# Optimization experiments

Hardware: AMD Instinct MI355X
Metric: run time of the kernel (lower is better)

The kernel has to match this reference:

```python
import jax, jax.numpy as jnp
import numpy as np

NUM_TREES = 256
DEPTH = 6
TREE_DIM = 2
INPUT_DIM = 256
BATCH = 2048


def sparsemax(x, axis=0):
    # Euclidean projection onto the simplex along `axis`.
    x = jnp.moveaxis(x, axis, -1)
    z = jnp.flip(jnp.sort(x, axis=-1), axis=-1)           # descending
    cz = jnp.cumsum(z, axis=-1)
    k = jnp.arange(1, x.shape[-1] + 1, dtype=x.dtype)
    support = (1.0 + k * z) > cz                          # boolean support set
    k_sel = jnp.sum(support, axis=-1, keepdims=True)      # |S(z)|
    tau = (jnp.take_along_axis(cz, k_sel - 1, axis=-1) - 1.0) / k_sel.astype(x.dtype)
    out = jnp.maximum(x - tau, 0.0)
    return jnp.moveaxis(out, -1, axis)


def sparsemoid(x):
    return jnp.clip(0.5 * x + 0.5, 0.0, 1.0)


def make_bin_codes(depth):
    idx = np.arange(2 ** depth)
    offs = 2 ** np.arange(depth)
    bc = ((idx[None, :] // offs[:, None]) % 2).astype(np.float32)  # [depth, 2^depth]
    return jnp.asarray(np.stack([bc, 1.0 - bc], axis=-1))          # [depth, 2^depth, 2]


def setup_inputs() -> dict:
    key = jax.random.key(0)
    ks = jax.random.split(key, 5)
    return {
        "inputs": jax.random.normal(ks[0], (BATCH, INPUT_DIM), dtype=jnp.float32),
        "feature_selection_logits": jax.random.normal(ks[1], (INPUT_DIM, NUM_TREES, DEPTH), dtype=jnp.float32),
        "feature_thresholds": jax.random.normal(ks[2], (NUM_TREES, DEPTH), dtype=jnp.float32) * 0.5,
        "log_temperatures": jax.random.normal(ks[3], (NUM_TREES, DEPTH), dtype=jnp.float32) * 0.1,
        "response": jax.random.normal(ks[4], (NUM_TREES, TREE_DIM, 2 ** DEPTH), dtype=jnp.float32),
    }


def reference(inputs, feature_selection_logits, feature_thresholds, log_temperatures, response):
    bin_codes_1hot = make_bin_codes(DEPTH)                                  # [d, 2^d, 2]
    selectors = sparsemax(feature_selection_logits, axis=0)                 # [i, n, d]
    feature_values = jnp.einsum('bi,ind->bnd', inputs, selectors)           # [b, n, d]
    tl = (feature_values - feature_thresholds) * jnp.exp(-log_temperatures) # [b, n, d]
    threshold_logits = jnp.stack([-tl, tl], axis=-1)                        # [b, n, d, 2]
    bins = sparsemoid(threshold_logits)                                     # [b, n, d, 2]
    bin_matches = jnp.einsum('bnds,dcs->bndc', bins, bin_codes_1hot)        # [b, n, d, 2^d]
    response_weights = jnp.prod(bin_matches, axis=-2)                       # [b, n, 2^d]
    out = jnp.einsum('bnc,ntc->bnt', response_weights, response)            # [b, n, tree_dim]
    return out.reshape(out.shape[0], -1)                                    # [b, n*tree_dim]
```

## Files before the change

kernel.cpp:

```cpp
#include <hip/hip_runtime.h>
#include <hip/hip_fp16.h>
#include <math.h>

#define NUM_TREES 256
#define DEPTH 6
#define TREE_DIM 2
#define INPUT_DIM 256
#define BATCH 2048
#define NLEAF 64
#define NCOLS (NUM_TREES * DEPTH)
#define KDIM INPUT_DIM

typedef _Float16 half8 __attribute__((ext_vector_type(8)));
typedef float floatx4 __attribute__((ext_vector_type(4)));

__global__ __launch_bounds__(256) void sparsemax_bisect(
    const float* __restrict__ fsl,
    const float* __restrict__ inputs,
    _Float16* __restrict__ selT,
    _Float16* __restrict__ inH)
{
    const int tid = threadIdx.x;
    {
        const int gid = blockIdx.x * 256 + tid;
        if (gid < (BATCH * INPUT_DIM) / 8) {
            const float4 v0 = ((const float4*)inputs)[gid * 2];
            const float4 v1 = ((const float4*)inputs)[gid * 2 + 1];
            half8 h;
            h[0] = (_Float16)v0.x; h[1] = (_Float16)v0.y;
            h[2] = (_Float16)v0.z; h[3] = (_Float16)v0.w;
            h[4] = (_Float16)v1.x; h[5] = (_Float16)v1.y;
            h[6] = (_Float16)v1.z; h[7] = (_Float16)v1.w;
            *(half8*)(inH + gid * 8) = h;
        }
    }

    const int lane = tid & 63;
    const int wave = tid >> 6;
    const int col  = blockIdx.x * 4 + wave;
    const int n = col / 6;
    const int d = col - n * 6;

    float x[4];
#pragma unroll
    for (int j = 0; j < 4; ++j)
        x[j] = fsl[(j * 64 + lane) * NCOLS + col];

    float mx = fmaxf(fmaxf(x[0], x[1]), fmaxf(x[2], x[3]));
#pragma unroll
    for (int off = 32; off > 0; off >>= 1)
        mx = fmaxf(mx, __shfl_xor(mx, off));

    float lo = mx - 1.0f, hi = mx;
    for (int it = 0; it < 16; ++it) {
        const float mid = 0.5f * (lo + hi);
        float s = fmaxf(x[0] - mid, 0.0f) + fmaxf(x[1] - mid, 0.0f)
                + fmaxf(x[2] - mid, 0.0f) + fmaxf(x[3] - mid, 0.0f);
#pragma unroll
        for (int off = 32; off > 0; off >>= 1)
            s += __shfl_xor(s, off);
        if (s > 1.0f) lo = mid; else hi = mid;
    }
    const float tau = 0.5f * (lo + hi);

    _Float16* dst = selT + (n * 8 + d) * KDIM;
#pragma unroll
    for (int j = 0; j < 4; ++j)
        dst[j * 64 + lane] = (_Float16)fmaxf(x[j] - tau, 0.0f);
}

#define BM 128
#define BN 64
#define BK 64
#define AP 72
#define BP 72
#define FVS 68

__global__ __launch_bounds__(256) void odt_mfma_kernel(
    const _Float16* __restrict__ inH,
    const _Float16* __restrict__ selT,
    const float* __restrict__ thr,
    const float* __restrict__ logt,
    const float* __restrict__ resp,
    float* __restrict__ out)
{
    __shared__ union {
        struct {
            _Float16 A[BM][AP];
            _Float16 B[BN][BP];
        } s;
        float fv[BM][FVS];
    } u;
    __shared__ float respS[8 * TREE_DIM * NLEAF];

    const int tid = threadIdx.x;
    const int b0 = blockIdx.x * BM;
    const int treeBase = blockIdx.y * 8;
    const int colBase  = blockIdx.y * BN;

    ((float4*)respS)[tid] = ((const float4*)(resp + treeBase * TREE_DIM * NLEAF))[tid];

    const int lane = tid & 63;
    const int w    = tid >> 6;
    const int wm   = w >> 1, wn = w & 1;
    const int l16  = lane & 15, quad = lane >> 4;

    floatx4 acc[4][2];
#pragma unroll
    for (int mt = 0; mt < 4; ++mt)
#pragma unroll
        for (int nt = 0; nt < 2; ++nt)
            acc[mt][nt] = (floatx4){0.f, 0.f, 0.f, 0.f};

    const int arow = tid >> 1, ahr = tid & 1;
    const int bcol = tid >> 2, bq  = tid & 3;

    for (int k0 = 0; k0 < KDIM; k0 += BK) {
        __syncthreads();
        {
            const _Float16* ag = inH + (b0 + arow) * KDIM + k0 + ahr * 32;
            const half8 a0 = *(const half8*)(ag);
            const half8 a1 = *(const half8*)(ag + 8);
            const half8 a2 = *(const half8*)(ag + 16);
            const half8 a3 = *(const half8*)(ag + 24);
            *(half8*)&u.s.A[arow][ahr * 32 + 0]  = a0;
            *(half8*)&u.s.A[arow][ahr * 32 + 8]  = a1;
            *(half8*)&u.s.A[arow][ahr * 32 + 16] = a2;
            *(half8*)&u.s.A[arow][ahr * 32 + 24] = a3;
        }
        {
            const _Float16* bg = selT + (colBase + bcol) * KDIM + k0 + bq * 16;
            const half8 b0v = *(const half8*)(bg);
            const half8 b1v = *(const half8*)(bg + 8);
            *(half8*)&u.s.B[bcol][bq * 16 + 0] = b0v;
            *(half8*)&u.s.B[bcol][bq * 16 + 8] = b1v;
        }
        __syncthreads();

#pragma unroll
        for (int h = 0; h < 2; ++h) {
            const half8 bf0 = *(const half8*)&u.s.B[wn * 32 + l16][quad * 8 + h * 32];
            const half8 bf1 = *(const half8*)&u.s.B[wn * 32 + 16 + l16][quad * 8 + h * 32];
#pragma unroll
            for (int mt = 0; mt < 4; ++mt) {
                const half8 af = *(const half8*)&u.s.A[wm * 64 + mt * 16 + l16][quad * 8 + h * 32];
                acc[mt][0] = __builtin_amdgcn_mfma_f32_16x16x32_f16(af, bf0, acc[mt][0], 0, 0, 0);
                acc[mt][1] = __builtin_amdgcn_mfma_f32_16x16x32_f16(af, bf1, acc[mt][1], 0, 0, 0);
            }
        }
    }

    __syncthreads();

#pragma unroll
    for (int mt = 0; mt < 4; ++mt)
#pragma unroll
        for (int nt = 0; nt < 2; ++nt)
#pragma unroll
            for (int r = 0; r < 4; ++r)
                u.fv[wm * 64 + mt * 16 + quad * 4 + r][wn * 32 + nt * 16 + l16] = acc[mt][nt][r];
    __syncthreads();

#pragma unroll
    for (int p = 0; p < 4; ++p) {
        const int idx = tid + 256 * p;
        const int row = idx & 127;
        const int tl  = idx >> 7;
        const int n   = treeBase + tl;
        const float* f = &u.fv[row][tl * 8];

        float sd[DEPTH];
#pragma unroll
        for (int d = 0; d < DEPTH; ++d) {
            const float tlg = (f[d] - thr[n * DEPTH + d]) * __expf(-logt[n * DEPTH + d]);
            sd[d] = fminf(fmaxf(0.5f + 0.5f * tlg, 0.0f), 1.0f);
        }
        float wv[NLEAF];
        wv[0] = 1.0f;
#pragma unroll
        for (int d = 0; d < DEPTH; ++d) {
            const int sz = 1 << d;
#pragma unroll
            for (int c2 = 0; c2 < NLEAF / 2; ++c2) {
                if (c2 < sz) {
                    const float t = wv[c2];
                    wv[c2]      = t * sd[d];
                    wv[c2 + sz] = t * (1.0f - sd[d]);
                }
            }
        }
        const float* r0 = &respS[tl * TREE_DIM * NLEAF];
        float o0 = 0.0f, o1 = 0.0f;
#pragma unroll
        for (int c2 = 0; c2 < NLEAF; ++c2) {
            o0 = fmaf(wv[c2], r0[c2], o0);
            o1 = fmaf(wv[c2], r0[NLEAF + c2], o1);
        }
        float2 o = {o0, o1};
        *(float2*)(out + (b0 + row) * (NUM_TREES * TREE_DIM) + n * TREE_DIM) = o;
    }
}

extern "C" void kernel_launch(void* const* d_in, const int* in_sizes, int n_in,
                              void* d_out, int out_size, void* d_ws, size_t ws_size,
                              hipStream_t stream) {
    const float* inputs = (const float*)d_in[0];
    const float* fsl    = (const float*)d_in[1];
    const float* thr    = (const float*)d_in[2];
    const float* logt   = (const float*)d_in[3];
    const float* resp   = (const float*)d_in[4];
    float* out = (float*)d_out;
    _Float16* selT = (_Float16*)d_ws;
    _Float16* inH  = (_Float16*)((char*)d_ws + (1 << 20));

    hipLaunchKernelGGL(sparsemax_bisect, dim3(NCOLS / 4), dim3(256), 0, stream,
                       fsl, inputs, selT, inH);
    hipLaunchKernelGGL(odt_mfma_kernel, dim3(BATCH / BM, NUM_TREES / 8), dim3(256),
                       0, stream, inH, selT, thr, logt, resp, out);
}
```

Before: 91.81 us.

## Halve GEMM M-tile, raise occupancy, and factor last tree level out of leaf sum

Cuts the batch tile from 128 to 64 rows and asks for 4 blocks per CU, which doubles the grid and lowers per-thread accumulator and epilogue registers. Global-to-LDS staging is unified so each thread loads 16 halves of both A and B. In the epilogue the leaf weights are built only for the first five depth levels (32 entries), and the sixth level's split is applied afterwards as two partial dot products, which halves the weight array and removes multiplies. The trade-off is less reuse of each B tile per block and more blocks to schedule.

Result: no change. 90.38 us (-1.6%).

```diff
diff --git a/kernel.cpp b/kernel.cpp
--- a/kernel.cpp
+++ b/kernel.cpp
@@ -69,14 +69,14 @@
         dst[j * 64 + lane] = (_Float16)fmaxf(x[j] - tau, 0.0f);
 }
 
-#define BM 128
+#define BM 64
 #define BN 64
 #define BK 64
 #define AP 72
 #define BP 72
 #define FVS 68
 
-__global__ __launch_bounds__(256) void odt_mfma_kernel(
+__global__ __launch_bounds__(256, 4) void odt_mfma_kernel(
     const _Float16* __restrict__ inH,
     const _Float16* __restrict__ selT,
     const float* __restrict__ thr,
@@ -105,35 +105,28 @@
     const int wm   = w >> 1, wn = w & 1;
     const int l16  = lane & 15, quad = lane >> 4;
 
-    floatx4 acc[4][2];
-#pragma unroll
-    for (int mt = 0; mt < 4; ++mt)
+    floatx4 acc[2][2];
+#pragma unroll
+    for (int mt = 0; mt < 2; ++mt)
 #pragma unroll
         for (int nt = 0; nt < 2; ++nt)
             acc[mt][nt] = (floatx4){0.f, 0.f, 0.f, 0.f};
 
-    const int arow = tid >> 1, ahr = tid & 1;
-    const int bcol = tid >> 2, bq  = tid & 3;
+    const int srow = tid >> 2, sseg = tid & 3;
 
     for (int k0 = 0; k0 < KDIM; k0 += BK) {
         __syncthreads();
         {
-            const _Float16* ag = inH + (b0 + arow) * KDIM + k0 + ahr * 32;
+            const _Float16* ag = inH + (b0 + srow) * KDIM + k0 + sseg * 16;
             const half8 a0 = *(const half8*)(ag);
             const half8 a1 = *(const half8*)(ag + 8);
-            const half8 a2 = *(const half8*)(ag + 16);
-            const half8 a3 = *(const half8*)(ag + 24);
-            *(half8*)&u.s.A[arow][ahr * 32 + 0]  = a0;
-            *(half8*)&u.s.A[arow][ahr * 32 + 8]  = a1;
-            *(half8*)&u.s.A[arow][ahr * 32 + 16] = a2;
-            *(half8*)&u.s.A[arow][ahr * 32 + 24] = a3;
-        }
-        {
-            const _Float16* bg = selT + (colBase + bcol) * KDIM + k0 + bq * 16;
-            const half8 b0v = *(const half8*)(bg);
-            const half8 b1v = *(const half8*)(bg + 8);
-            *(half8*)&u.s.B[bcol][bq * 16 + 0] = b0v;
-            *(half8*)&u.s.B[bcol][bq * 16 + 8] = b1v;
+            *(half8*)&u.s.A[srow][sseg * 16 + 0] = a0;
+            *(half8*)&u.s.A[srow][sseg * 16 + 8] = a1;
+            const _Float16* bg = selT + (colBase + srow) * KDIM + k0 + sseg * 16;
+            const half8 bv0 = *(const half8*)(bg);
+            const half8 bv1 = *(const half8*)(bg + 8);
+            *(half8*)&u.s.B[srow][sseg * 16 + 0] = bv0;
+            *(half8*)&u.s.B[srow][sseg * 16 + 8] = bv1;
         }
         __syncthreads();
 
@@ -141,31 +134,31 @@
         for (int h = 0; h < 2; ++h) {
             const half8 bf0 = *(const half8*)&u.s.B[wn * 32 + l16][quad * 8 + h * 32];
             const half8 bf1 = *(const half8*)&u.s.B[wn * 32 + 16 + l16][quad * 8 + h * 32];
-#pragma unroll
-            for (int mt = 0; mt < 4; ++mt) {
-                const half8 af = *(const half8*)&u.s.A[wm * 64 + mt * 16 + l16][quad * 8 + h * 32];
-                acc[mt][0] = __builtin_amdgcn_mfma_f32_16x16x32_f16(af, bf0, acc[mt][0], 0, 0, 0);
-                acc[mt][1] = __builtin_amdgcn_mfma_f32_16x16x32_f16(af, bf1, acc[mt][1], 0, 0, 0);
-            }
+            const half8 af0 = *(const half8*)&u.s.A[wm * 32 + l16][quad * 8 + h * 32];
+            const half8 af1 = *(const half8*)&u.s.A[wm * 32 + 16 + l16][quad * 8 + h * 32];
+            acc[0][0] = __builtin_amdgcn_mfma_f32_16x16x32_f16(af0, bf0, acc[0][0], 0, 0, 0);
+            acc[0][1] = __builtin_amdgcn_mfma_f32_16x16x32_f16(af0, bf1, acc[0][1], 0, 0, 0);
+            acc[1][0] = __builtin_amdgcn_mfma_f32_16x16x32_f16(af1, bf0, acc[1][0], 0, 0, 0);
+            acc[1][1] = __builtin_amdgcn_mfma_f32_16x16x32_f16(af1, bf1, acc[1][1], 0, 0, 0);
         }
     }
 
     __syncthreads();
 
 #pragma unroll
-    for (int mt = 0; mt < 4; ++mt)
+    for (int mt = 0; mt < 2; ++mt)
 #pragma unroll
         for (int nt = 0; nt < 2; ++nt)
 #pragma unroll
             for (int r = 0; r < 4; ++r)
-                u.fv[wm * 64 + mt * 16 + quad * 4 + r][wn * 32 + nt * 16 + l16] = acc[mt][nt][r];
+                u.fv[wm * 32 + mt * 16 + quad * 4 + r][wn * 32 + nt * 16 + l16] = acc[mt][nt][r];
     __syncthreads();
 
 #pragma unroll
-    for (int p = 0; p < 4; ++p) {
+    for (int p = 0; p < 2; ++p) {
         const int idx = tid + 256 * p;
-        const int row = idx & 127;
-        const int tl  = idx >> 7;
+        const int row = idx & 63;
+        const int tl  = idx >> 6;
         const int n   = treeBase + tl;
         const float* f = &u.fv[row][tl * 8];
 
@@ -175,13 +168,13 @@
             const float tlg = (f[d] - thr[n * DEPTH + d]) * __expf(-logt[n * DEPTH + d]);
             sd[d] = fminf(fmaxf(0.5f + 0.5f * tlg, 0.0f), 1.0f);
         }
-        float wv[NLEAF];
+        float wv[NLEAF / 2];
         wv[0] = 1.0f;
 #pragma unroll
-        for (int d = 0; d < DEPTH; ++d) {
+        for (int d = 0; d < 5; ++d) {
             const int sz = 1 << d;
 #pragma unroll
-            for (int c2 = 0; c2 < NLEAF / 2; ++c2) {
+            for (int c2 = 0; c2 < 16; ++c2) {
                 if (c2 < sz) {
                     const float t = wv[c2];
                     wv[c2]      = t * sd[d];
@@ -190,13 +183,18 @@
             }
         }
         const float* r0 = &respS[tl * TREE_DIM * NLEAF];
-        float o0 = 0.0f, o1 = 0.0f;
-#pragma unroll
-        for (int c2 = 0; c2 < NLEAF; ++c2) {
-            o0 = fmaf(wv[c2], r0[c2], o0);
-            o1 = fmaf(wv[c2], r0[NLEAF + c2], o1);
-        }
-        float2 o = {o0, o1};
+        float a0 = 0.f, b0s = 0.f, a1 = 0.f, b1s = 0.f;
+#pragma unroll
+        for (int c2 = 0; c2 < 32; ++c2) {
+            a0  = fmaf(wv[c2], r0[c2], a0);
+            b0s = fmaf(wv[c2], r0[c2 + 32], b0s);
+            a1  = fmaf(wv[c2], r0[NLEAF + c2], a1);
+            b1s = fmaf(wv[c2], r0[NLEAF + c2 + 32], b1s);
+        }
+        const float s5 = sd[5], s5b = 1.0f - sd[5];
+        float2 o;
+        o.x = s5 * a0 + s5b * b0s;
+        o.y = s5 * a1 + s5b * b1s;
         *(float2*)(out + (b0 + row) * (NUM_TREES * TREE_DIM) + n * TREE_DIM) = o;
     }
 }
```
